# Kernel tuning notes

Measured on AMD Instinct MI355X. Metric: run time of the kernel, lower is better.

The kernel has to match this reference:

```python
import jax, jax.numpy as jnp
import numpy as np

T, B, N_INP, N_HID, N_OUT = 512, 512, 64, 768, 64
DT = 0.01


def setup_inputs() -> dict:
    key = jax.random.key(0)
    k = jax.random.split(key, 7)
    d_in = N_INP + 2 * N_HID  # 1600, concat(x, hz, hy)
    s = lambda fan_in: 1.0 / np.sqrt(fan_in)
    return {
        "x": jax.random.normal(k[0], (T, B, N_INP), dtype=jnp.float32),
        "W_h": jax.random.uniform(k[1], (N_HID, d_in), jnp.float32, -s(d_in), s(d_in)),
        "b_h": jax.random.uniform(k[2], (N_HID,), jnp.float32, -s(d_in), s(d_in)),
        "W_p": jax.random.uniform(k[3], (N_HID, d_in), jnp.float32, -s(d_in), s(d_in)),
        "b_p": jax.random.uniform(k[4], (N_HID,), jnp.float32, -s(d_in), s(d_in)),
        "W_r": jax.random.uniform(k[5], (N_OUT, N_HID), jnp.float32, -s(N_HID), s(N_HID)),
        "b_r": jax.random.uniform(k[6], (N_OUT,), jnp.float32, -s(N_HID), s(N_HID)),
    }


def reference(x, W_h, b_h, W_p, b_p, W_r, b_r):
    dt = jnp.asarray(DT, x.dtype)

    def step(carry, xt):
        hy, hz, hp = carry
        # |.|**2 == square for real inputs
        sq = jnp.concatenate([jnp.square(xt), jnp.square(hz), jnp.square(hy)], axis=1)
        hp = jnp.tanh(sq @ W_p.T + b_p)
        lin = jnp.concatenate([xt, hz, hy], axis=1)
        hz = hz + dt * (jnp.tanh(lin @ W_h.T + b_h) + hp)
        hy = hy + dt * hz
        return (hy, hz, hp), None

    h0 = jnp.zeros((x.shape[1], N_HID), x.dtype)
    (hy, hz, hp), _ = jax.lax.scan(step, (h0, h0, h0), x)
    return hy @ W_r.T + b_r
```

## Files before the change

### kernel.cpp

```cpp
#include <hip/hip_runtime.h>
#include <hip/hip_fp16.h>

typedef _Float16 f16x8 __attribute__((ext_vector_type(8)));
typedef float f32x4 __attribute__((ext_vector_type(4)));
typedef float f32x16 __attribute__((ext_vector_type(16)));
typedef unsigned short u16;
typedef unsigned int u32;

#define T_STEPS 512
#define BATCH   512
#define DTF     0.01f

#define CTR_OFF 0
#define CTR_SZ  1048576
#define WB_OFF  (CTR_OFF + CTR_SZ)
#define WB_SZ   (32*200*384*2)
#define WRB_OFF (WB_OFF + WB_SZ)
#define WRB_SZ  (4*24*64*8*2)
#define ST_OFF  (WRB_OFF + WRB_SZ)
#define ST_SZ   (2*8*64*1536*2)
#define WS_NEED (ST_OFF + ST_SZ)

#define MFMA32(a,b,c) __builtin_amdgcn_mfma_f32_32x32x16_f16((a),(b),(c),0,0,0)
#define MFMA16(a,b,c) __builtin_amdgcn_mfma_f32_16x16x32_f16((a),(b),(c),0,0,0)

#define ACQUIRE_L1() asm volatile("s_waitcnt vmcnt(0)\n\tbuffer_inv sc0" ::: "memory")

__device__ __forceinline__ u16 f2h(float f){ _Float16 h = (_Float16)f; return *reinterpret_cast<u16*>(&h); }

__device__ __forceinline__ float ftanh(float x){
  float a = fminf(fmaxf(x, -12.f), 12.f);
  float e = __expf(2.f * a);
  return 1.f - 2.f * __builtin_amdgcn_rcpf(e + 1.f);
}


__global__ __launch_bounds__(64) void prep_weights(const float* __restrict__ Wh,
                                                   const float* __restrict__ Wp,
                                                   const float* __restrict__ Wr,
                                                   u16* __restrict__ Wb, u16* __restrict__ Wrb){
  int b = blockIdx.x, l = threadIdx.x;
  if (b < 6400){
    int s = b / 200, r2 = b % 200;
    int m2 = r2 / 100, u = r2 % 100;
    if (l < 48){
      int c = l >> 1, kh = l & 1;
      int gg = c*2 + kh, rr = gg >> 3, cc = gg & 7;
      size_t dst = (size_t)s*76800 + (size_t)(m2*100 + u)*384 + (size_t)rr*64 + (size_t)((cc ^ (rr & 7))*8);
      const float* W = m2 ? Wp : Wh;
      const float* src = W + (size_t)(s*24 + c)*1600 + u*16 + kh*8;
      f16x8 o;
#pragma unroll
      for (int e = 0; e < 8; ++e) o[e] = (_Float16)src[e];
      *reinterpret_cast<f16x8*>(Wb + dst) = o;
    }
  } else {
    int b2 = b - 6400;
    int nt = b2 / 24, kt = b2 % 24;
    int c = nt*16 + (l & 15), k = kt*32 + (l >> 4)*8;
    const float* src = Wr + (size_t)c*768 + k;
    f16x8 o;
#pragma unroll
    for (int e = 0; e < 8; ++e) o[e] = (_Float16)src[e];
    *reinterpret_cast<f16x8*>(Wrb + ((size_t)b2*64 + l)*8) = o;
  }
}

__global__ __launch_bounds__(256, 1) void rnn_main(
    const float* __restrict__ x, const float* __restrict__ bh_g, const float* __restrict__ bp_g,
    const float* __restrict__ br_g, const u16* __restrict__ Wb, const u16* __restrict__ Wrb,
    u16* __restrict__ st, u32* __restrict__ ctr, float* __restrict__ out)
{
  __shared__ float scr[6144];
  __shared__ int s_dead, s_slot, s_xcd;

  const int tid = threadIdx.x;
  if (tid == 0){
    s_dead = 0;
    u32 xcd;
    asm volatile("s_getreg_b32 %0, hwreg(HW_REG_XCC_ID)" : "=s"(xcd));
    xcd &= 7u;
    s_xcd  = (int)xcd;
    s_slot = (int)atomicAdd(ctr + xcd, 1u);
  }
  __syncthreads();
  const int gx = s_xcd;
  const int s  = s_slot;
  if (s >= 32) return;

  const int c0   = s * 24;
  const int l    = tid & 63;
  const int wv   = tid >> 6;
  const bool matH = (wv < 2);
  const int p    = wv & 1;
  const int colW = l & 31;
  const int khB  = l >> 5;
  const bool validC = (colW < 24);
  const int colB = validC ? colW : colW - 24;
  const int gran = colB*2 + khB;
  const int grr  = gran >> 3, gcc = gran & 7;
  const int bfi  = grr*8 + (gcc ^ (grr & 7));

  u32* FL = ctr + 2048 + (size_t)gx*16384;

  f16x8 Bv[50];
  {
    const f16x8* WBg = reinterpret_cast<const f16x8*>(Wb);
    const size_t base = (size_t)s*9600 + (size_t)(((matH ? 0 : 100) + (p ? 50 : 0)))*48 + bfi;
#pragma unroll
    for (int u = 0; u < 50; ++u) Bv[u] = WBg[base + (size_t)u*48];
  }

  const int dcol = c0 + (validC ? colW : 0);
  float bhv = 0.f, bpv = 0.f;
  if (wv < 2){ bhv = bh_g[dcol]; bpv = bp_g[dcol]; }

  float hz[16] = {}, hy[16] = {};

  auto wait_flags = [&](u32 tgt){
    if (s_dead) return;
    long spins = 0;
    for (;;){
      bool ok = true;
      if (l < 32) ok = (__hip_atomic_load(FL + l*32, __ATOMIC_RELAXED, __HIP_MEMORY_SCOPE_AGENT) >= tgt);
      if (__all(ok)) break;
      __builtin_amdgcn_s_sleep(1);
      if (++spins > 1000000L){ if (l == 0) s_dead = 1; break; }
    }
  };

#define SLOOP(U0c, NUc, DOSQ, BOFF) do { \
    f16x8 av0[4], av1[4]; \
    _Pragma("unroll") \
    for (int j = 0; j < 4; ++j){ \
      av0[j] = *reinterpret_cast<const f16x8*>(stb0 + (size_t)((U0c)-4+j)*16); \
      av1[j] = *reinterpret_cast<const f16x8*>(stb1 + (size_t)((U0c)-4+j)*16); \
    } \
    _Pragma("unroll") \
    for (int i = 0; i < (NUc); ++i){ \
      f16x8 a0 = av0[i&3], a1 = av1[i&3]; \
      if (i + 4 < (NUc)){ \
        av0[i&3] = *reinterpret_cast<const f16x8*>(stb0 + (size_t)((U0c)+i)*16); \
        av1[i&3] = *reinterpret_cast<const f16x8*>(stb1 + (size_t)((U0c)+i)*16); \
      } \
      if (DOSQ){ a0 = a0*a0; a1 = a1*a1; } \
      acc0 = MFMA32(a0, Bv[(BOFF)+i], acc0); \
      acc1 = MFMA32(a1, Bv[(BOFF)+i], acc1); \
    } } while (0)

#pragma unroll 1
  for (int t = 0; t < T_STEPS; ++t){
    f16x8 xa0[4], xa1[4];
    if (p == 0){
#pragma unroll
      for (int mm = 0; mm < 2; ++mm){
        const float* xb = x + ((size_t)t*BATCH + gx*64 + mm*32 + colW)*64 + khB*8;
#pragma unroll
        for (int u = 0; u < 4; ++u){
          const float4 uu = *reinterpret_cast<const float4*>(xb + u*16);
          const float4 vv = *reinterpret_cast<const float4*>(xb + u*16 + 4);
          f16x8 r;
          if (matH){
            r[0]=(_Float16)uu.x; r[1]=(_Float16)uu.y; r[2]=(_Float16)uu.z; r[3]=(_Float16)uu.w;
            r[4]=(_Float16)vv.x; r[5]=(_Float16)vv.y; r[6]=(_Float16)vv.z; r[7]=(_Float16)vv.w;
          } else {
            r[0]=(_Float16)(uu.x*uu.x); r[1]=(_Float16)(uu.y*uu.y); r[2]=(_Float16)(uu.z*uu.z); r[3]=(_Float16)(uu.w*uu.w);
            r[4]=(_Float16)(vv.x*vv.x); r[5]=(_Float16)(vv.y*vv.y); r[6]=(_Float16)(vv.z*vv.z); r[7]=(_Float16)(vv.w*vv.w);
          }
          if (mm) xa1[u] = r; else xa0[u] = r;
        }
      }
    }

    if (wv == 0){
      if (t > 0) wait_flags((u32)t);
      ACQUIRE_L1();
    }
    __syncthreads();
    if (s_dead) break;

    const u16* stb0 = st + ((((size_t)(t&1)*8 + gx)*64) + colW)*1536 + khB*8;
    const u16* stb1 = stb0 + (size_t)32*1536;

    f32x16 acc0 = {}, acc1 = {};
    if (p == 0){
#pragma unroll
      for (int u = 0; u < 4; ++u){
        acc0 = MFMA32(xa0[u], Bv[u], acc0);
        acc1 = MFMA32(xa1[u], Bv[u], acc1);
      }
      if (matH) SLOOP(4, 46, 0, 4); else SLOOP(4, 46, 1, 4);
    } else {
      if (matH) SLOOP(50, 50, 0, 0); else SLOOP(50, 50, 1, 0);
    }

    if (wv == 0){
#pragma unroll
      for (int e = 0; e < 16; ++e) scr[3*1024 + e*64 + l] = acc1[e];
    } else if (wv == 1){
#pragma unroll
      for (int e = 0; e < 16; ++e) scr[0*1024 + e*64 + l] = acc0[e];
    } else if (wv == 2){
#pragma unroll
      for (int e = 0; e < 16; ++e){ scr[1*1024 + e*64 + l] = acc0[e];
                                    scr[4*1024 + e*64 + l] = acc1[e]; }
    } else {
#pragma unroll
      for (int e = 0; e < 16; ++e){ scr[2*1024 + e*64 + l] = acc0[e];
                                    scr[5*1024 + e*64 + l] = acc1[e]; }
    }
    __syncthreads();

    if (wv < 2){
      const int rH = wv ? 3 : 0;
      const int rP = wv ? 4 : 1;
      u16* wtb = st + (((size_t)((t+1)&1)*8 + gx)*64)*1536;
      const int mrow = wv*32;
#pragma unroll
      for (int e = 0; e < 16; ++e){
        float aH = (wv ? acc1[e] : acc0[e]) + scr[rH*1024 + e*64 + l];
        float aP = scr[rP*1024 + e*64 + l] + scr[(rP+1)*1024 + e*64 + l];
        float hv = ftanh(aH + bhv);
        float pv = ftanh(aP + bpv);
        hz[e] += DTF * (hv + pv);
        hy[e] += DTF * hz[e];
        if (validC){
          int row = mrow + (e & 3) + 8*(e >> 2) + 4*khB;
          wtb[(size_t)row*1536 + dcol]       = f2h(hz[e]);
          wtb[(size_t)row*1536 + 768 + dcol] = f2h(hy[e]);
        }
      }
      asm volatile("s_waitcnt vmcnt(0)" ::: "memory");
    }
    __syncthreads();
    if (tid == 0)
      __hip_atomic_store(FL + s*32, (u32)(t+1), __ATOMIC_RELAXED, __HIP_MEMORY_SCOPE_AGENT);
  }
#undef SLOOP

  if (s == 0 && !s_dead){
    if (wv == 0){ wait_flags((u32)T_STEPS); ACQUIRE_L1(); }
    __syncthreads();
    if (!s_dead){
      const int colL = l & 15, kq4 = l >> 4;
      const u16* hyb = st + (((size_t)gx*64) + wv*16 + colL)*1536 + 768 + kq4*8;
      const f16x8* Wr8 = reinterpret_cast<const f16x8*>(Wrb);
      f32x4 oc[4] = {};
#pragma unroll
      for (int kt = 0; kt < 24; ++kt){
        f16x8 a = *reinterpret_cast<const f16x8*>(hyb + (size_t)kt*32);
#pragma unroll
        for (int nt = 0; nt < 4; ++nt)
          oc[nt] = MFMA16(a, Wr8[(nt*24 + kt)*64 + l], oc[nt]);
      }
      const int rowC = wv*16 + kq4*4;
#pragma unroll
      for (int nt = 0; nt < 4; ++nt){
        float bb = br_g[nt*16 + colL];
#pragma unroll
        for (int e = 0; e < 4; ++e)
          out[(size_t)(gx*64 + rowC + e)*64 + nt*16 + colL] = oc[nt][e] + bb;
      }
    }
  }
}

extern "C" void kernel_launch(void* const* d_in, const int* in_sizes, int n_in,
                              void* d_out, int out_size, void* d_ws, size_t ws_size,
                              hipStream_t stream) {
  const float* x  = (const float*)d_in[0];
  const float* Wh = (const float*)d_in[1];
  const float* bh = (const float*)d_in[2];
  const float* Wp = (const float*)d_in[3];
  const float* bp = (const float*)d_in[4];
  const float* Wr = (const float*)d_in[5];
  const float* br = (const float*)d_in[6];
  float* out = (float*)d_out;

  if (ws_size < (size_t)WS_NEED) return;
  char* ws = (char*)d_ws;

  u16* Wb  = (u16*)(ws + WB_OFF);
  u16* Wrb = (u16*)(ws + WRB_OFF);
  u16* st  = (u16*)(ws + ST_OFF);
  u32* ctr = (u32*)(ws + CTR_OFF);

  hipMemsetAsync(ws + CTR_OFF, 0, CTR_SZ, stream);
  hipMemsetAsync(ws + ST_OFF,  0, ST_SZ,  stream);

  prep_weights<<<6496, 64, 0, stream>>>(Wh, Wp, Wr, Wb, Wrb);

  rnn_main<<<256, 256, 0, stream>>>(x, bh, bp, br, Wb, Wrb, st, ctr, out);
}
```

Measured before the change: 8.142 ms.

## Split K reduction across eight waves per block instead of four

Doubles the workgroup to 512 threads and splits each matrix's K dimension (100 fragments) across four waves instead of two, so each wave holds only 25 weight fragments in registers and does fewer MFMAs per step. Partial sums are reduced through a larger dynamic shared-memory scratch (16 regions). This shortens the per-step serial MFMA chain on the recurrent critical path, at the cost of more LDS traffic and reduction adds per step.

```diff
diff --git a/kernel.cpp b/kernel.cpp
--- a/kernel.cpp
+++ b/kernel.cpp
@@ -66,13 +66,14 @@
   }
 }
 
-__global__ __launch_bounds__(256, 1) void rnn_main(
+__global__ __launch_bounds__(512, 1) void rnn_main(
     const float* __restrict__ x, const float* __restrict__ bh_g, const float* __restrict__ bp_g,
     const float* __restrict__ br_g, const u16* __restrict__ Wb, const u16* __restrict__ Wrb,
     u16* __restrict__ st, u32* __restrict__ ctr, float* __restrict__ out)
 {
-  __shared__ float scr[6144];
+  extern __shared__ u16 smem[];
   __shared__ int s_dead, s_slot, s_xcd;
+  float* scr = reinterpret_cast<float*>(smem);
 
   const int tid = threadIdx.x;
   if (tid == 0){
@@ -91,8 +92,8 @@
   const int c0   = s * 24;
   const int l    = tid & 63;
   const int wv   = tid >> 6;
-  const bool matH = (wv < 2);
-  const int p    = wv & 1;
+  const int q    = wv >> 1;
+  const int matP = wv & 1;
   const int colW = l & 31;
   const int khB  = l >> 5;
   const bool validC = (colW < 24);
@@ -103,12 +104,12 @@
 
   u32* FL = ctr + 2048 + (size_t)gx*16384;
 
-  f16x8 Bv[50];
+  f16x8 Bv[25];
   {
     const f16x8* WBg = reinterpret_cast<const f16x8*>(Wb);
-    const size_t base = (size_t)s*9600 + (size_t)(((matH ? 0 : 100) + (p ? 50 : 0)))*48 + bfi;
-#pragma unroll
-    for (int u = 0; u < 50; ++u) Bv[u] = WBg[base + (size_t)u*48];
+    const size_t base = (size_t)s*9600 + (size_t)((matP ? 100 : 0) + q*25)*48 + bfi;
+#pragma unroll
+    for (int j = 0; j < 25; ++j) Bv[j] = WBg[base + (size_t)j*48];
   }
 
   const int dcol = c0 + (validC ? colW : 0);
@@ -129,29 +130,31 @@
     }
   };
 
-#define SLOOP(U0c, NUc, DOSQ, BOFF) do { \
+#define RG(mI,matI,qI) ((((mI)*2 + (matI))*4 + (qI))*1024)
+
+#define SLOOP(OFF0c, NUc, BOFFc, DOSQc) do { \
     f16x8 av0[4], av1[4]; \
     _Pragma("unroll") \
     for (int j = 0; j < 4; ++j){ \
-      av0[j] = *reinterpret_cast<const f16x8*>(stb0 + (size_t)((U0c)-4+j)*16); \
-      av1[j] = *reinterpret_cast<const f16x8*>(stb1 + (size_t)((U0c)-4+j)*16); \
+      av0[j] = *reinterpret_cast<const f16x8*>(stb0 + (size_t)((OFF0c)+j)*16); \
+      av1[j] = *reinterpret_cast<const f16x8*>(stb1 + (size_t)((OFF0c)+j)*16); \
     } \
     _Pragma("unroll") \
     for (int i = 0; i < (NUc); ++i){ \
       f16x8 a0 = av0[i&3], a1 = av1[i&3]; \
       if (i + 4 < (NUc)){ \
-        av0[i&3] = *reinterpret_cast<const f16x8*>(stb0 + (size_t)((U0c)+i)*16); \
-        av1[i&3] = *reinterpret_cast<const f16x8*>(stb1 + (size_t)((U0c)+i)*16); \
+        av0[i&3] = *reinterpret_cast<const f16x8*>(stb0 + (size_t)((OFF0c)+i+4)*16); \
+        av1[i&3] = *reinterpret_cast<const f16x8*>(stb1 + (size_t)((OFF0c)+i+4)*16); \
       } \
-      if (DOSQ){ a0 = a0*a0; a1 = a1*a1; } \
-      acc0 = MFMA32(a0, Bv[(BOFF)+i], acc0); \
-      acc1 = MFMA32(a1, Bv[(BOFF)+i], acc1); \
+      if (DOSQc){ a0 = a0*a0; a1 = a1*a1; } \
+      acc0 = MFMA32(a0, Bv[(BOFFc)+i], acc0); \
+      acc1 = MFMA32(a1, Bv[(BOFFc)+i], acc1); \
     } } while (0)
 
 #pragma unroll 1
   for (int t = 0; t < T_STEPS; ++t){
     f16x8 xa0[4], xa1[4];
-    if (p == 0){
+    if (q == 0){
 #pragma unroll
       for (int mm = 0; mm < 2; ++mm){
         const float* xb = x + ((size_t)t*BATCH + gx*64 + mm*32 + colW)*64 + khB*8;
@@ -160,7 +163,7 @@
           const float4 uu = *reinterpret_cast<const float4*>(xb + u*16);
           const float4 vv = *reinterpret_cast<const float4*>(xb + u*16 + 4);
           f16x8 r;
-          if (matH){
+          if (!matP){
             r[0]=(_Float16)uu.x; r[1]=(_Float16)uu.y; r[2]=(_Float16)uu.z; r[3]=(_Float16)uu.w;
             r[4]=(_Float16)vv.x; r[5]=(_Float16)vv.y; r[6]=(_Float16)vv.z; r[7]=(_Float16)vv.w;
           } else {
@@ -183,43 +186,46 @@
     const u16* stb1 = stb0 + (size_t)32*1536;
 
     f32x16 acc0 = {}, acc1 = {};
-    if (p == 0){
+    if (q == 0){
 #pragma unroll
       for (int u = 0; u < 4; ++u){
         acc0 = MFMA32(xa0[u], Bv[u], acc0);
         acc1 = MFMA32(xa1[u], Bv[u], acc1);
       }
-      if (matH) SLOOP(4, 46, 0, 4); else SLOOP(4, 46, 1, 4);
+      if (!matP) SLOOP(0, 21, 4, 0); else SLOOP(0, 21, 4, 1);
     } else {
-      if (matH) SLOOP(50, 50, 0, 0); else SLOOP(50, 50, 1, 0);
+      const int off0 = q*25 - 4;
+      if (!matP) SLOOP(off0, 25, 0, 0); else SLOOP(off0, 25, 0, 1);
     }
 
     if (wv == 0){
 #pragma unroll
-      for (int e = 0; e < 16; ++e) scr[3*1024 + e*64 + l] = acc1[e];
+      for (int e = 0; e < 16; ++e) scr[RG(1,0,0) + e*64 + l] = acc1[e];
     } else if (wv == 1){
 #pragma unroll
-      for (int e = 0; e < 16; ++e) scr[0*1024 + e*64 + l] = acc0[e];
-    } else if (wv == 2){
-#pragma unroll
-      for (int e = 0; e < 16; ++e){ scr[1*1024 + e*64 + l] = acc0[e];
-                                    scr[4*1024 + e*64 + l] = acc1[e]; }
+      for (int e = 0; e < 16; ++e) scr[RG(0,1,0) + e*64 + l] = acc0[e];
     } else {
 #pragma unroll
-      for (int e = 0; e < 16; ++e){ scr[2*1024 + e*64 + l] = acc0[e];
-                                    scr[5*1024 + e*64 + l] = acc1[e]; }
+      for (int e = 0; e < 16; ++e){
+        scr[RG(0,matP,q) + e*64 + l] = acc0[e];
+        scr[RG(1,matP,q) + e*64 + l] = acc1[e];
+      }
     }
     __syncthreads();
 
     if (wv < 2){
-      const int rH = wv ? 3 : 0;
-      const int rP = wv ? 4 : 1;
       u16* wtb = st + (((size_t)((t+1)&1)*8 + gx)*64)*1536;
       const int mrow = wv*32;
 #pragma unroll
       for (int e = 0; e < 16; ++e){
-        float aH = (wv ? acc1[e] : acc0[e]) + scr[rH*1024 + e*64 + l];
-        float aP = scr[rP*1024 + e*64 + l] + scr[(rP+1)*1024 + e*64 + l];
+        float aH, aP;
+        if (wv == 0){
+          aH = acc0[e] + scr[RG(0,0,1)+e*64+l] + scr[RG(0,0,2)+e*64+l] + scr[RG(0,0,3)+e*64+l];
+          aP = scr[RG(0,1,0)+e*64+l] + scr[RG(0,1,1)+e*64+l] + scr[RG(0,1,2)+e*64+l] + scr[RG(0,1,3)+e*64+l];
+        } else {
+          aP = acc1[e] + scr[RG(1,1,1)+e*64+l] + scr[RG(1,1,2)+e*64+l] + scr[RG(1,1,3)+e*64+l];
+          aH = scr[RG(1,0,0)+e*64+l] + scr[RG(1,0,1)+e*64+l] + scr[RG(1,0,2)+e*64+l] + scr[RG(1,0,3)+e*64+l];
+        }
         float hv = ftanh(aH + bhv);
         float pv = ftanh(aP + bpv);
         hz[e] += DTF * (hv + pv);
@@ -237,11 +243,12 @@
       __hip_atomic_store(FL + s*32, (u32)(t+1), __ATOMIC_RELAXED, __HIP_MEMORY_SCOPE_AGENT);
   }
 #undef SLOOP
+#undef RG
 
   if (s == 0 && !s_dead){
     if (wv == 0){ wait_flags((u32)T_STEPS); ACQUIRE_L1(); }
     __syncthreads();
-    if (!s_dead){
+    if (!s_dead && wv < 4){
       const int colL = l & 15, kq4 = l >> 4;
       const u16* hyb = st + (((size_t)gx*64) + wv*16 + colL)*1536 + 768 + kq4*8;
       const f16x8* Wr8 = reinterpret_cast<const f16x8*>(Wrb);
@@ -290,5 +297,7 @@
 
   prep_weights<<<6496, 64, 0, stream>>>(Wh, Wp, Wr, Wb, Wrb);
 
-  rnn_main<<<256, 256, 0, stream>>>(x, bh, bp, br, Wb, Wrb, st, ctr, out);
+  (void)hipFuncSetAttribute(reinterpret_cast<const void*>(rnn_main),
+                            hipFuncAttributeMaxDynamicSharedMemorySize, 90112);
+  rnn_main<<<256, 512, 90112, stream>>>(x, bh, bp, br, Wb, Wrb, st, ctr, out);
 }
```

New measurement: 8.827 ms. +8.4%, slower.

## Move per-block weight slice from registers into LDS and serialize reduction exchange

Applied to the files above, without the earlier changes.

Weights that were held in 50 f16x8 registers per lane are now copied once into dynamic shared memory (about 150 KB) and read from LDS for each MFMA. This frees a large share of the register file, which goes to a deeper 8-deep prefetch of state operands. Because the weights now fill most of LDS, the cross-wave reduction scratch is cut to two 4 KB buffers reused across several extra __syncthreads phases. The cost is added LDS read traffic on every MFMA and more barriers per timestep on a latency-bound recurrent loop.

```diff
diff --git a/kernel.cpp b/kernel.cpp
--- a/kernel.cpp
+++ b/kernel.cpp
@@ -71,7 +71,7 @@
     const float* __restrict__ br_g, const u16* __restrict__ Wb, const u16* __restrict__ Wrb,
     u16* __restrict__ st, u32* __restrict__ ctr, float* __restrict__ out)
 {
-  __shared__ float scr[6144];
+  extern __shared__ u16 smem[];
   __shared__ int s_dead, s_slot, s_xcd;
 
   const int tid = threadIdx.x;
@@ -91,7 +91,7 @@
   const int c0   = s * 24;
   const int l    = tid & 63;
   const int wv   = tid >> 6;
-  const bool matH = (wv < 2);
+  const int matP = wv >> 1;
   const int p    = wv & 1;
   const int colW = l & 31;
   const int khB  = l >> 5;
@@ -103,13 +103,16 @@
 
   u32* FL = ctr + 2048 + (size_t)gx*16384;
 
-  f16x8 Bv[50];
   {
-    const f16x8* WBg = reinterpret_cast<const f16x8*>(Wb);
-    const size_t base = (size_t)s*9600 + (size_t)(((matH ? 0 : 100) + (p ? 50 : 0)))*48 + bfi;
-#pragma unroll
-    for (int u = 0; u < 50; ++u) Bv[u] = WBg[base + (size_t)u*48];
-  }
+    const float4* srcw = reinterpret_cast<const float4*>(Wb + (size_t)s*76800);
+    float4* dst = reinterpret_cast<float4*>(smem);
+    for (int i = tid; i < 9600; i += 256) dst[i] = srcw[i];
+  }
+  __syncthreads();
+
+  const f16x8* WBp = reinterpret_cast<const f16x8*>(smem);
+  float* scr = reinterpret_cast<float*>(smem + 76800);
+  const int mb = matP*100;
 
   const int dcol = c0 + (validC ? colW : 0);
   float bhv = 0.f, bpv = 0.f;
@@ -129,23 +132,24 @@
     }
   };
 
-#define SLOOP(U0c, NUc, DOSQ, BOFF) do { \
-    f16x8 av0[4], av1[4]; \
+#define SLOOP(U0c, NUc, DOSQc) do { \
+    f16x8 av0[8], av1[8]; \
     _Pragma("unroll") \
-    for (int j = 0; j < 4; ++j){ \
+    for (int j = 0; j < 8; ++j){ \
       av0[j] = *reinterpret_cast<const f16x8*>(stb0 + (size_t)((U0c)-4+j)*16); \
       av1[j] = *reinterpret_cast<const f16x8*>(stb1 + (size_t)((U0c)-4+j)*16); \
     } \
     _Pragma("unroll") \
     for (int i = 0; i < (NUc); ++i){ \
-      f16x8 a0 = av0[i&3], a1 = av1[i&3]; \
-      if (i + 4 < (NUc)){ \
-        av0[i&3] = *reinterpret_cast<const f16x8*>(stb0 + (size_t)((U0c)+i)*16); \
-        av1[i&3] = *reinterpret_cast<const f16x8*>(stb1 + (size_t)((U0c)+i)*16); \
+      f16x8 b8 = WBp[(mb + (U0c) + i)*48 + bfi]; \
+      f16x8 a0 = av0[i&7], a1 = av1[i&7]; \
+      if (i + 8 < (NUc)){ \
+        av0[i&7] = *reinterpret_cast<const f16x8*>(stb0 + (size_t)((U0c)+4+i)*16); \
+        av1[i&7] = *reinterpret_cast<const f16x8*>(stb1 + (size_t)((U0c)+4+i)*16); \
       } \
-      if (DOSQ){ a0 = a0*a0; a1 = a1*a1; } \
-      acc0 = MFMA32(a0, Bv[(BOFF)+i], acc0); \
-      acc1 = MFMA32(a1, Bv[(BOFF)+i], acc1); \
+      if (DOSQc){ a0 = a0*a0; a1 = a1*a1; } \
+      acc0 = MFMA32(a0, b8, acc0); \
+      acc1 = MFMA32(a1, b8, acc1); \
     } } while (0)
 
 #pragma unroll 1
@@ -160,7 +164,7 @@
           const float4 uu = *reinterpret_cast<const float4*>(xb + u*16);
           const float4 vv = *reinterpret_cast<const float4*>(xb + u*16 + 4);
           f16x8 r;
-          if (matH){
+          if (!matP){
             r[0]=(_Float16)uu.x; r[1]=(_Float16)uu.y; r[2]=(_Float16)uu.z; r[3]=(_Float16)uu.w;
             r[4]=(_Float16)vv.x; r[5]=(_Float16)vv.y; r[6]=(_Float16)vv.z; r[7]=(_Float16)vv.w;
           } else {
@@ -186,42 +190,66 @@
     if (p == 0){
 #pragma unroll
       for (int u = 0; u < 4; ++u){
-        acc0 = MFMA32(xa0[u], Bv[u], acc0);
-        acc1 = MFMA32(xa1[u], Bv[u], acc1);
-      }
-      if (matH) SLOOP(4, 46, 0, 4); else SLOOP(4, 46, 1, 4);
+        f16x8 b8 = WBp[(mb + u)*48 + bfi];
+        acc0 = MFMA32(xa0[u], b8, acc0);
+        acc1 = MFMA32(xa1[u], b8, acc1);
+      }
+      if (!matP) SLOOP(4, 46, 0); else SLOOP(4, 46, 1);
     } else {
-      if (matH) SLOOP(50, 50, 0, 0); else SLOOP(50, 50, 1, 0);
-    }
-
+      if (!matP) SLOOP(50, 50, 0); else SLOOP(50, 50, 1);
+    }
+
+    float aH[16], aP[16];
+    if (wv == 1){
+#pragma unroll
+      for (int e = 0; e < 16; ++e) scr[e*64 + l] = acc0[e];
+    } else if (wv == 0){
+#pragma unroll
+      for (int e = 0; e < 16; ++e) scr[1024 + e*64 + l] = acc1[e];
+    }
+    __syncthreads();
     if (wv == 0){
 #pragma unroll
-      for (int e = 0; e < 16; ++e) scr[3*1024 + e*64 + l] = acc1[e];
+      for (int e = 0; e < 16; ++e) aH[e] = acc0[e] + scr[e*64 + l];
     } else if (wv == 1){
 #pragma unroll
-      for (int e = 0; e < 16; ++e) scr[0*1024 + e*64 + l] = acc0[e];
+      for (int e = 0; e < 16; ++e) aH[e] = acc1[e] + scr[1024 + e*64 + l];
+    }
+    __syncthreads();
+    if (wv == 2){
+#pragma unroll
+      for (int e = 0; e < 16; ++e) scr[e*64 + l] = acc0[e];
+    } else if (wv == 3){
+#pragma unroll
+      for (int e = 0; e < 16; ++e) scr[1024 + e*64 + l] = acc1[e];
+    }
+    __syncthreads();
+    if (wv == 0){
+#pragma unroll
+      for (int e = 0; e < 16; ++e) aP[e] = scr[e*64 + l];
+    } else if (wv == 1){
+#pragma unroll
+      for (int e = 0; e < 16; ++e) aP[e] = scr[1024 + e*64 + l];
+    }
+    __syncthreads();
+    if (wv == 3){
+#pragma unroll
+      for (int e = 0; e < 16; ++e) scr[e*64 + l] = acc0[e];
     } else if (wv == 2){
 #pragma unroll
-      for (int e = 0; e < 16; ++e){ scr[1*1024 + e*64 + l] = acc0[e];
-                                    scr[4*1024 + e*64 + l] = acc1[e]; }
-    } else {
-#pragma unroll
-      for (int e = 0; e < 16; ++e){ scr[2*1024 + e*64 + l] = acc0[e];
-                                    scr[5*1024 + e*64 + l] = acc1[e]; }
+      for (int e = 0; e < 16; ++e) scr[1024 + e*64 + l] = acc1[e];
     }
     __syncthreads();
 
     if (wv < 2){
-      const int rH = wv ? 3 : 0;
-      const int rP = wv ? 4 : 1;
       u16* wtb = st + (((size_t)((t+1)&1)*8 + gx)*64)*1536;
       const int mrow = wv*32;
+      const int rbase = wv ? 1024 : 0;
 #pragma unroll
       for (int e = 0; e < 16; ++e){
-        float aH = (wv ? acc1[e] : acc0[e]) + scr[rH*1024 + e*64 + l];
-        float aP = scr[rP*1024 + e*64 + l] + scr[(rP+1)*1024 + e*64 + l];
-        float hv = ftanh(aH + bhv);
-        float pv = ftanh(aP + bpv);
+        float aPf = aP[e] + scr[rbase + e*64 + l];
+        float hv = ftanh(aH[e] + bhv);
+        float pv = ftanh(aPf + bpv);
         hz[e] += DTF * (hv + pv);
         hy[e] += DTF * hz[e];
         if (validC){
@@ -290,5 +318,7 @@
 
   prep_weights<<<6496, 64, 0, stream>>>(Wh, Wp, Wr, Wb, Wrb);
 
-  rnn_main<<<256, 256, 0, stream>>>(x, bh, bp, br, Wb, Wrb, st, ctr, out);
+  (void)hipFuncSetAttribute(reinterpret_cast<const void*>(rnn_main),
+                            hipFuncAttributeMaxDynamicSharedMemorySize, 161792);
+  rnn_main<<<256, 256, 161792, stream>>>(x, bh, bp, br, Wb, Wrb, st, ctr, out);
 }
```

Measured after the change: 7.768 ms. 1.05x faster.
